# Optimization experiments

Measured on AMD Instinct MI355X. Metric: run time of the kernel, lower is better.

The kernel has to match this reference:

```python
import jax, jax.numpy as jnp
import numpy as np

HH = 38  # sqrt(amd0=1444)
KD = 3   # 3x3 neighborhood


def setup_inputs() -> dict:
    key = jax.random.key(0)
    fm = jax.random.normal(key, (16, 512, HH, HH), dtype=jnp.float32)
    return {"fm": fm}


def reference(fm):
    # fm: [B, C, H, W] -> replication pad 1 -> NHWC -> gather 3x3 neighbors,
    # concatenated along the channel axis in row-major neighbor order
    # (matching counts[:, 0..8] = (h-1,w-1),(h-1,w),(h-1,w+1),(h,w-1),...).
    B, C, H, W = fm.shape
    x = jnp.pad(fm, ((0, 0), (0, 0), (1, 1), (1, 1)), mode="edge")  # [B,C,H+2,W+2]
    x = jnp.transpose(x, (0, 2, 3, 1))  # [B, H+2, W+2, C]
    patches = [x[:, di:di + H, dj:dj + W, :] for di in range(KD) for dj in range(KD)]
    pfm = jnp.concatenate(patches, axis=-1)  # [B, H, W, 9*C]
    return pfm.reshape(B, H * W, KD * KD * C)  # [B, 1444, 9*C]
```

## Files before the change

kernel.cpp:

```cpp
#include <hip/hip_runtime.h>


#define BB 16
#define CC 512
#define HH 38
#define WW 38
#define HW (HH * WW)
#define KK 9
#define CCH 128
#define NCH (CC / CCH)
#define LSTRIDE 39
#define NTHREADS 512

__global__ __launch_bounds__(NTHREADS) void spatial_pool_kernel(
    const float* __restrict__ fm, float* __restrict__ out)
{
    __shared__ float lds[3][CCH][LSTRIDE];

    const int blk   = blockIdx.x;
    const int chunk = blk & (NCH - 1);
    const int bh    = blk >> 2;
    const int h     = bh % HH;
    const int b     = bh / HH;
    const int c0    = chunk * CCH;

    const int r0 = (h - 1 < 0) ? 0 : h - 1;
    const int r1 = h;
    const int r2 = (h + 1 > HH - 1) ? HH - 1 : h + 1;

    const float* base = fm + ((size_t)b * CC + c0) * HW;
    const int NLOAD = 3 * CCH * WW;
    for (int idx = threadIdx.x; idx < NLOAD; idx += NTHREADS) {
        int w  = idx % WW;
        int rc = idx / WW;
        int c  = rc & (CCH - 1);
        int r  = rc >> 7;
        int hr = (r == 0) ? r0 : ((r == 1) ? r1 : r2);
        lds[r][c][w] = base[c * HW + hr * WW + w];
    }
    __syncthreads();

    float* outb = out + (((size_t)b * HW + (size_t)h * WW) * KK) * CC + c0;
    const int NST = WW * KK * CCH;
    for (int i = threadIdx.x; i < NST; i += NTHREADS) {
        int c  = i & (CCH - 1);
        int wk = i >> 7;
        int w  = wk / KK;
        int k  = wk - w * KK;
        int di = k / 3;
        int dj = k - di * 3;
        int wp = w + dj - 1;
        wp = (wp < 0) ? 0 : ((wp > WW - 1) ? WW - 1 : wp);
        outb[(size_t)wk * CC + c] = lds[di][c][wp];
    }
}

extern "C" void kernel_launch(void* const* d_in, const int* in_sizes, int n_in,
                              void* d_out, int out_size, void* d_ws, size_t ws_size,
                              hipStream_t stream) {
    const float* fm = (const float*)d_in[0];
    float* out = (float*)d_out;
    dim3 grid(BB * HH * NCH);
    dim3 block(NTHREADS);
    spatial_pool_kernel<<<grid, block, 0, stream>>>(fm, out);
}
```

Baseline: 471.5 us.

## Replace LDS gather with per-input scatter to all nine output slots

Rewrites the kernel from an output-centric gather through shared memory to an input-centric scatter. Each thread loads up to four consecutive width pixels of one channel with float2 reads and writes each value directly to all output positions that reference it, replication edges included, using nontemporal stores. The LDS staging and block barrier are gone, and the grid becomes finer with 256-thread blocks. The cost is input reads strided by HW across threads, so reads coalesce poorly, and each block now covers only a few pixels.

```diff
diff --git a/kernel.cpp b/kernel.cpp
--- a/kernel.cpp
+++ b/kernel.cpp
@@ -7,51 +7,69 @@
 #define WW 38
 #define HW (HH * WW)
 #define KK 9
-#define CCH 128
-#define NCH (CC / CCH)
-#define LSTRIDE 39
-#define NTHREADS 512
+#define NT 256
+#define NW4 10
 
-__global__ __launch_bounds__(NTHREADS) void spatial_pool_kernel(
+__global__ __launch_bounds__(NT) void spatial_pool_scatter(
     const float* __restrict__ fm, float* __restrict__ out)
 {
-    __shared__ float lds[3][CCH][LSTRIDE];
-
     const int blk   = blockIdx.x;
-    const int chunk = blk & (NCH - 1);
-    const int bh    = blk >> 2;
+    const int w4    = blk % NW4;
+    const int t     = blk / NW4;
+    const int chalf = t & 1;
+    const int bh    = t >> 1;
     const int h     = bh % HH;
     const int b     = bh / HH;
-    const int c0    = chunk * CCH;
+    const int c     = chalf * NT + threadIdx.x;
 
-    const int r0 = (h - 1 < 0) ? 0 : h - 1;
-    const int r1 = h;
-    const int r2 = (h + 1 > HH - 1) ? HH - 1 : h + 1;
+    const int w0 = w4 * 4;
+    const int nw = (w4 == NW4 - 1) ? 2 : 4;
 
-    const float* base = fm + ((size_t)b * CC + c0) * HW;
-    const int NLOAD = 3 * CCH * WW;
-    for (int idx = threadIdx.x; idx < NLOAD; idx += NTHREADS) {
-        int w  = idx % WW;
-        int rc = idx / WW;
-        int c  = rc & (CCH - 1);
-        int r  = rc >> 7;
-        int hr = (r == 0) ? r0 : ((r == 1) ? r1 : r2);
-        lds[r][c][w] = base[c * HW + hr * WW + w];
+    const float* src = fm + ((size_t)(b * CC + c)) * HW + h * WW + w0;
+    float v[4];
+    {
+        float2 r0 = *(const float2*)src;
+        v[0] = r0.x; v[1] = r0.y;
+        if (nw == 4) {
+            float2 r1 = *(const float2*)(src + 2);
+            v[2] = r1.x; v[3] = r1.y;
+        }
     }
-    __syncthreads();
 
-    float* outb = out + (((size_t)b * HW + (size_t)h * WW) * KK) * CC + c0;
-    const int NST = WW * KK * CCH;
-    for (int i = threadIdx.x; i < NST; i += NTHREADS) {
-        int c  = i & (CCH - 1);
-        int wk = i >> 7;
-        int w  = wk / KK;
-        int k  = wk - w * KK;
-        int di = k / 3;
-        int dj = k - di * 3;
-        int wp = w + dj - 1;
-        wp = (wp < 0) ? 0 : ((wp > WW - 1) ? WW - 1 : wp);
-        outb[(size_t)wk * CC + c] = lds[di][c][wp];
+    int hrow[3];
+    {
+        int n = 0;
+        #pragma unroll
+        for (int di = 0; di < 3; ++di) {
+            int hm = h + 1 - di;
+            if (0 <= hm && hm < HH) { hrow[n] = (b * HW + hm * WW) * KK + di * 3; n++; }
+        }
+        if (h == 0)      { hrow[n] = (b * HW) * KK; n++; }
+        if (h == HH - 1) { hrow[n] = (b * HW + (HH - 1) * WW) * KK + 6; n++; }
+    }
+
+    for (int wi = 0; wi < nw; ++wi) {
+        const int w = w0 + wi;
+        int woff[3];
+        {
+            int m = 0;
+            #pragma unroll
+            for (int dj = 0; dj < 3; ++dj) {
+                int wm = w + 1 - dj;
+                if (0 <= wm && wm < WW) { woff[m] = wm * KK + dj; m++; }
+            }
+            if (w == 0)      { woff[m] = 0; m++; }
+            if (w == WW - 1) { woff[m] = (WW - 1) * KK + 2; m++; }
+        }
+        const float val = v[wi];
+        #pragma unroll
+        for (int i = 0; i < 3; ++i) {
+            #pragma unroll
+            for (int j = 0; j < 3; ++j) {
+                unsigned idx = (unsigned)(hrow[i] + woff[j]) * (unsigned)CC + (unsigned)c;
+                __builtin_nontemporal_store(val, out + (size_t)idx);
+            }
+        }
     }
 }
 
@@ -60,7 +78,7 @@
                               hipStream_t stream) {
     const float* fm = (const float*)d_in[0];
     float* out = (float*)d_out;
-    dim3 grid(BB * HH * NCH);
-    dim3 block(NTHREADS);
-    spatial_pool_kernel<<<grid, block, 0, stream>>>(fm, out);
+    dim3 grid(NW4 * 2 * BB * HH);
+    dim3 block(NT);
+    spatial_pool_scatter<<<grid, block, 0, stream>>>(fm, out);
 }
```

Result: no change. 462.6 us (-1.9%).
